# Performance work log

Measured on AMD Instinct MI355X. Metric: run time of the kernel, lower is better.

Reference implementation:

```python
import jax, jax.numpy as jnp
import numpy as np

B, T, D = 2, 2048, 1024
N_HEADS = 16
HEAD_DIM = D // N_HEADS
HIDDEN = 4 * D
LN_EPS = 1e-6  # flax LayerNorm default


def apply_rotary_pos_emb(x, positions):
    # x: (B, T, H, head_dim); positions: (T,)
    head_dim = x.shape[-1]
    inv_freq = 1.0 / 10000 ** (jnp.arange(0, head_dim, 2).astype(jnp.float32) / head_dim)
    freqs = jnp.outer(positions.astype(jnp.float32), inv_freq)  # (T, head_dim//2)
    cos_emb = jnp.cos(freqs)[None, :, None, :]
    sin_emb = jnp.sin(freqs)[None, :, None, :]
    x1 = x[..., : head_dim // 2]
    x2 = x[..., head_dim // 2 :]
    return jnp.concatenate([x1 * cos_emb - x2 * sin_emb,
                            x1 * sin_emb + x2 * cos_emb], axis=-1)


def layernorm(x, scale, bias):
    mu = jnp.mean(x, axis=-1, keepdims=True)
    var = jnp.mean(jnp.square(x - mu), axis=-1, keepdims=True)
    return (x - mu) * jax.lax.rsqrt(var + LN_EPS) * scale + bias


def setup_inputs() -> dict:
    key = jax.random.key(0)
    ks = jax.random.split(key, 8)
    lecun = lambda k, shape: jax.random.normal(k, shape, jnp.float32) * (1.0 / np.sqrt(shape[0]))
    x = jax.random.normal(ks[0], (B, T, D), jnp.float32)
    positions = jnp.arange(T, dtype=jnp.int32)
    mask = jnp.tril(jnp.ones((T, T), dtype=bool))[None, None]  # causal (1,1,T,T)
    return {
        "x": x,
        "positions": positions,
        "mask": mask,
        "ln1_scale": jnp.ones((D,), jnp.float32),
        "ln1_bias": jnp.zeros((D,), jnp.float32),
        "w_qkv": lecun(ks[1], (D, 3 * D)),
        "w_o": lecun(ks[2], (D, D)),
        "ln2_scale": jnp.ones((D,), jnp.float32),
        "ln2_bias": jnp.zeros((D,), jnp.float32),
        "w1": lecun(ks[3], (D, HIDDEN)),
        "b1": jnp.zeros((HIDDEN,), jnp.float32),
        "w2": lecun(ks[4], (HIDDEN, D)),
        "b2": jnp.zeros((D,), jnp.float32),
    }


def reference(x, positions, mask, ln1_scale, ln1_bias, w_qkv, w_o,
              ln2_scale, ln2_bias, w1, b1, w2, b2):
    h = layernorm(x, ln1_scale, ln1_bias)
    qkv = h @ w_qkv  # (B,T,3D)
    qkv = qkv.reshape(B, T, 3, N_HEADS, HEAD_DIM)
    q, k, v = jnp.moveaxis(qkv, 2, 0)  # each (B,T,H,hd)
    q = apply_rotary_pos_emb(q, positions)
    k = apply_rotary_pos_emb(k, positions)
    q = jnp.transpose(q, (0, 2, 1, 3))  # (B,H,T,hd)
    k = jnp.transpose(k, (0, 2, 1, 3))
    v = jnp.transpose(v, (0, 2, 1, 3))
    scale = 1.0 / jnp.sqrt(jnp.float32(HEAD_DIM))
    attn_weights = jnp.einsum('bhqd,bhkd->bhqk', q, k) * scale
    attn_weights = jnp.where(mask, attn_weights, -1e10)
    attn_weights = jax.nn.softmax(attn_weights, axis=-1)
    h = jnp.einsum('bhqk,bhkd->bhqd', attn_weights, v)
    h = jnp.transpose(h, (0, 2, 1, 3)).reshape(B, T, D)
    h = h @ w_o
    x = x + h
    h = layernorm(x, ln2_scale, ln2_bias)
    h = jax.nn.gelu(h @ w1 + b1)  # approximate gelu, matching flax nn.gelu default
    h = h @ w2 + b2
    return x + h
```

## Files before the change

### kernel.cpp

```cpp
#include <hip/hip_runtime.h>


typedef __bf16 bf16_t;
typedef bf16_t bf16x8 __attribute__((ext_vector_type(8)));
typedef float f32x4 __attribute__((ext_vector_type(4)));

#define M_ROWS 4096
#define DMODEL 1024
#define TSEQ   2048
#define NHEAD  16
#define HDIM   64

__device__ __forceinline__ ushort f2bf(float f) {
  union { float f; unsigned u; } v; v.f = f;
  unsigned r = (v.u + 0x7fffu + ((v.u >> 16) & 1u)) >> 16;
  return (ushort)r;
}
__device__ __forceinline__ float bf2f(ushort u) {
  union { unsigned u; float f; } v; v.u = ((unsigned)u) << 16;
  return v.f;
}
__device__ __forceinline__ unsigned cvt_pk_bf16(float a, float b) {
  unsigned r;
  asm("v_cvt_pk_bf16_f32 %0, %1, %2" : "=v"(r) : "v"(a), "v"(b));
  return r;
}
__device__ __forceinline__ void gload_lds16(const void* g, void* l) {
  __builtin_amdgcn_global_load_lds(
      (const __attribute__((address_space(1))) unsigned*)g,
      (__attribute__((address_space(3))) unsigned*)l, 16, 0, 0);
}
__device__ __forceinline__ f32x4 mfma16(bf16x8 a, bf16x8 b, f32x4 c) {
  return __builtin_amdgcn_mfma_f32_16x16x32_bf16(a, b, c, 0, 0, 0);
}
__device__ __forceinline__ float gelu_f(float x) {
  float y = 0.7978845608028654f * (x + 0.044715f * x * x * x);
  float e = __expf(2.0f * y);
  float t = 1.0f - 2.0f / (e + 1.0f);
  return 0.5f * x * (1.0f + t);
}

__global__ __launch_bounds__(256)
void transpose_bf16(const float* __restrict__ src, ushort* __restrict__ dst,
                    int K, int N) {
  __shared__ float t[32][33];
  int n0 = blockIdx.x * 32, k0 = blockIdx.y * 32;
  int tx = threadIdx.x & 31, ty = threadIdx.x >> 5;
#pragma unroll
  for (int i = 0; i < 4; i++) {
    int k = ty + i * 8;
    t[k][tx] = src[(size_t)(k0 + k) * N + n0 + tx];
  }
  __syncthreads();
#pragma unroll
  for (int i = 0; i < 4; i++) {
    int nn = ty + i * 8;
    dst[(size_t)(n0 + nn) * K + k0 + tx] = f2bf(t[tx][nn]);
  }
}

__global__ __launch_bounds__(256)
void ln_kernel(const float* __restrict__ x, const float* __restrict__ sc,
               const float* __restrict__ bi, ushort* __restrict__ out) {
  int row = blockIdx.x;
  int tid = threadIdx.x;
  const float4 v = *(const float4*)&x[(size_t)row * DMODEL + tid * 4];
  float s = v.x + v.y + v.z + v.w;
  float s2 = v.x * v.x + v.y * v.y + v.z * v.z + v.w * v.w;
#pragma unroll
  for (int off = 32; off > 0; off >>= 1) {
    s += __shfl_down(s, off);
    s2 += __shfl_down(s2, off);
  }
  __shared__ float red[8];
  int lane = tid & 63, w = tid >> 6;
  if (lane == 0) { red[w * 2] = s; red[w * 2 + 1] = s2; }
  __syncthreads();
  float S = red[0] + red[2] + red[4] + red[6];
  float S2 = red[1] + red[3] + red[5] + red[7];
  float mu = S * (1.0f / DMODEL);
  float var = S2 * (1.0f / DMODEL) - mu * mu;
  float rs = rsqrtf(var + 1e-6f);
  float4 scv = *(const float4*)&sc[tid * 4];
  float4 biv = *(const float4*)&bi[tid * 4];
  ushort4 o;
  o.x = f2bf((v.x - mu) * rs * scv.x + biv.x);
  o.y = f2bf((v.y - mu) * rs * scv.y + biv.y);
  o.z = f2bf((v.z - mu) * rs * scv.z + biv.z);
  o.w = f2bf((v.w - mu) * rs * scv.w + biv.w);
  *(ushort4*)&out[(size_t)row * DMODEL + tid * 4] = o;
}

__global__ __launch_bounds__(256)
void rope_table(const int* __restrict__ positions, float2* __restrict__ tab) {
  int i = blockIdx.x * 256 + threadIdx.x;
  int t = i >> 5, f = i & 31;
  float inv = __expf(-(float)f * (1.0f / 32.0f) * 9.210340371976184f);
  float a = (float)positions[t] * inv;
  tab[i] = make_float2(cosf(a), sinf(a));
}

__global__ __launch_bounds__(256)
void rope_apply(const ushort* __restrict__ qkv, const float2* __restrict__ tab,
                ushort* __restrict__ Q, ushort* __restrict__ Kd,
                ushort* __restrict__ VT) {
  __shared__ ushort vt[64][66];
  int t0 = blockIdx.x * 64;
  int bh = blockIdx.y;
  int b = bh >> 4, h = bh & 15;
  int f = threadIdx.x & 31, tg = threadIdx.x >> 5;
#pragma unroll
  for (int i = 0; i < 8; i++) {
    int tt = tg * 8 + i;
    int t = t0 + tt;
    const ushort* qr = qkv + (size_t)(b * TSEQ + t) * 3072 + h * 64 + f;
    float2 cs = tab[t * 32 + f];
    float c = cs.x, s = cs.y;
    float q1 = bf2f(qr[0]),    q2 = bf2f(qr[32]);
    float k1 = bf2f(qr[1024]), k2 = bf2f(qr[1056]);
    ushort* Qp = Q + ((size_t)bh * TSEQ + t) * HDIM;
    ushort* Kp = Kd + ((size_t)bh * TSEQ + t) * HDIM;
    Qp[f]      = f2bf(q1 * c - q2 * s);
    Qp[f + 32] = f2bf(q1 * s + q2 * c);
    Kp[f]      = f2bf(k1 * c - k2 * s);
    Kp[f + 32] = f2bf(k1 * s + k2 * c);
    vt[f][tt]      = qr[2048];
    vt[f + 32][tt] = qr[2080];
  }
  __syncthreads();
  int t = threadIdx.x & 63, fg = threadIdx.x >> 6;
  ushort* Vp = VT + (size_t)bh * HDIM * TSEQ + t0 + t;
#pragma unroll
  for (int j = 0; j < 16; j++) {
    int ff = fg * 16 + j;
    Vp[(size_t)ff * TSEQ] = vt[ff][t];
  }
}

__global__ __launch_bounds__(256, 4)
void attn_kernel(const ushort* __restrict__ Q, const ushort* __restrict__ Kd,
                 const ushort* __restrict__ VT, ushort* __restrict__ O) {
  int bh = blockIdx.x;
  int qb = 31 - (int)blockIdx.y;
  int nt = qb + 1;
  int tid = threadIdx.x;
  int lane = tid & 63, w = tid >> 6;
  int qw = qb * 64 + w * 16;
  int lr = lane & 15, lg = lane >> 4;
  int q_abs = qw + lr;

  const ushort* Qb = Q + (size_t)bh * TSEQ * HDIM;
  const ushort* Kb = Kd + (size_t)bh * TSEQ * HDIM;
  const ushort* Vb = VT + (size_t)bh * HDIM * TSEQ;

  __shared__ ushort lK[2][64 * 64];
  __shared__ ushort lV[2][64 * 64];
  __shared__ ushort pt[4][16 * 64];
  ushort* myp = pt[w];

  int srow0 = tid >> 3, sch = tid & 7;

  auto stage = [&](int buf, int kt) {
#pragma unroll
    for (int c = 0; c < 2; c++) {
      int r = c * 32 + srow0;
      int gch = sch ^ (r & 7);
      gload_lds16(Kb + (size_t)(kt + r) * HDIM + gch * 8,
                  &lK[buf][c * 2048 + tid * 8]);
      gload_lds16(Vb + (size_t)r * TSEQ + kt + gch * 8,
                  &lV[buf][c * 2048 + tid * 8]);
    }
  };

  const float QS = 0.125f * 1.44269504088896340736f;
  bf16x8 aq0 = *(const bf16x8*)&Qb[(size_t)q_abs * HDIM + lg * 8];
  bf16x8 aq1 = *(const bf16x8*)&Qb[(size_t)q_abs * HDIM + 32 + lg * 8];
#pragma unroll
  for (int j = 0; j < 8; j++) {
    aq0[j] = (bf16_t)((float)aq0[j] * QS);
    aq1[j] = (bf16_t)((float)aq1[j] * QS);
  }

  float m_run = -1e30f, l_run = 0.0f;
  f32x4 o[4] = {};

  stage(0, 0);
  __syncthreads();

  for (int it = 0; it < nt; ++it) {
    int kt = it * 64;
    int buf = it & 1;
    bool diag = (it == nt - 1);

    if (it + 1 < nt) stage(buf ^ 1, kt + 64);

    f32x4 sa[4];
#pragma unroll
    for (int cb = 0; cb < 4; cb++) {
      int row = cb * 16 + lr;
      const ushort* kp = &lK[buf][row * 64];
      bf16x8 k0 = *(const bf16x8*)(kp + (((lg    ) ^ (row & 7)) << 3));
      bf16x8 k1 = *(const bf16x8*)(kp + (((lg + 4) ^ (row & 7)) << 3));
      f32x4 z = {};
      z = mfma16(k0, aq0, z);
      sa[cb] = mfma16(k1, aq1, z);
    }

    if (diag) {
#pragma unroll
      for (int cb = 0; cb < 4; cb++)
#pragma unroll
        for (int r = 0; r < 4; r++)
          if (kt + cb * 16 + lg * 4 + r > q_abs) sa[cb][r] = -1e30f;
    }

    f32x4 m4;
#pragma unroll
    for (int r = 0; r < 4; r++)
      m4[r] = fmaxf(fmaxf(sa[0][r], sa[1][r]), fmaxf(sa[2][r], sa[3][r]));
    float mx = fmaxf(fmaxf(m4[0], m4[1]), fmaxf(m4[2], m4[3]));
    mx = fmaxf(mx, __shfl_xor(mx, 16, 64));
    mx = fmaxf(mx, __shfl_xor(mx, 32, 64));
    float mn = fmaxf(m_run, mx);
    float rescale = __builtin_amdgcn_exp2f(m_run - mn);
    m_run = mn;

    float ps = 0.0f;
    uint2 pk[4];
#pragma unroll
    for (int cb = 0; cb < 4; cb++) {
      float p0 = __builtin_amdgcn_exp2f(sa[cb][0] - mn);
      float p1 = __builtin_amdgcn_exp2f(sa[cb][1] - mn);
      float p2 = __builtin_amdgcn_exp2f(sa[cb][2] - mn);
      float p3 = __builtin_amdgcn_exp2f(sa[cb][3] - mn);
      ps += (p0 + p1) + (p2 + p3);
      pk[cb].x = cvt_pk_bf16(p0, p1);
      pk[cb].y = cvt_pk_bf16(p2, p3);
    }
    ps += __shfl_xor(ps, 16, 64);
    ps += __shfl_xor(ps, 32, 64);
    l_run = l_run * rescale + ps;

#pragma unroll
    for (int cb = 0; cb < 4; cb++)
      *(uint2*)&myp[lr * 64 + (((cb * 4 + lg) ^ lr) << 2)] = pk[cb];

#pragma unroll
    for (int d = 0; d < 4; d++)
#pragma unroll
      for (int r = 0; r < 4; r++) o[d][r] *= rescale;

    union U8 { uint2 h[2]; bf16x8 v; };
    U8 t0, t1;
    t0.h[0] = *(const uint2*)&myp[lr * 64 + (((lg * 2    ) ^ lr) << 2)];
    t0.h[1] = *(const uint2*)&myp[lr * 64 + (((lg * 2 + 1) ^ lr) << 2)];
    t1.h[0] = *(const uint2*)&myp[lr * 64 + (((8 + lg * 2    ) ^ lr) << 2)];
    t1.h[1] = *(const uint2*)&myp[lr * 64 + (((8 + lg * 2 + 1) ^ lr) << 2)];

#pragma unroll
    for (int d = 0; d < 4; d++) {
      int row = d * 16 + lr;
      const ushort* vp = &lV[buf][row * 64];
      bf16x8 va0 = *(const bf16x8*)(vp + (((lg    ) ^ (row & 7)) << 3));
      bf16x8 va1 = *(const bf16x8*)(vp + (((lg + 4) ^ (row & 7)) << 3));
      o[d] = mfma16(va0, t0.v, o[d]);
      o[d] = mfma16(va1, t1.v, o[d]);
    }

    __syncthreads();
  }

  int b = bh >> 4, h = bh & 15;
  float linv = 1.0f / l_run;
  size_t obase = (size_t)(b * TSEQ + qw + lr) * DMODEL + h * 64;
#pragma unroll
  for (int d = 0; d < 4; d++) {
    uint2 st;
    st.x = cvt_pk_bf16(o[d][0] * linv, o[d][1] * linv);
    st.y = cvt_pk_bf16(o[d][2] * linv, o[d][3] * linv);
    *(uint2*)&O[obase + d * 16 + lg * 4] = st;
  }
}

template <int EPI, int BN>
__global__ __launch_bounds__(256)
void gemm_kernel(const ushort* __restrict__ A, const ushort* __restrict__ Bt,
                 void* __restrict__ Cout, const float* __restrict__ bias,
                 const float* __restrict__ resid, int M, int N, int K,
                 int nbn) {
  constexpr int NF = BN / 32;
  __shared__ ushort lA[128 * 64];
  __shared__ ushort lB[BN * 64];
  int tid = threadIdx.x;
  int lane = tid & 63, w = tid >> 6;
  int wm = w >> 1, wn = w & 1;

  int nwg = gridDim.x;
  int cpx = nwg >> 3;
  int wg = ((int)blockIdx.x & 7) * cpx + ((int)blockIdx.x >> 3);
  int bm = wg / nbn, bn = wg % nbn;

  f32x4 acc[4][NF] = {};

  const ushort* Ab = A + (size_t)bm * 128 * K;
  const ushort* Bb = Bt + (size_t)bn * BN * K;
  int lrow = lane & 15, lg = lane >> 4;
  int srow = tid >> 3, sch = tid & 7;

  for (int k0 = 0; k0 < K; k0 += 64) {
    __syncthreads();
#pragma unroll
    for (int c = 0; c < 4; c++) {
      int r = c * 32 + srow;
      int gch = sch ^ (r & 7);
      gload_lds16(Ab + (size_t)r * K + k0 + gch * 8, &lA[c * 2048 + tid * 8]);
    }
#pragma unroll
    for (int c = 0; c < BN / 32; c++) {
      int r = c * 32 + srow;
      int gch = sch ^ (r & 7);
      gload_lds16(Bb + (size_t)r * K + k0 + gch * 8, &lB[c * 2048 + tid * 8]);
    }
    __syncthreads();

    bf16x8 af[4], bfr[NF];
#pragma unroll
    for (int m = 0; m < 4; m++) {
      int row = wm * 64 + m * 16 + lrow;
      af[m] = *(const bf16x8*)&lA[row * 64 + ((lg ^ (row & 7)) << 3)];
    }
#pragma unroll
    for (int n = 0; n < NF; n++) {
      int row = wn * (BN / 2) + n * 16 + lrow;
      bfr[n] = *(const bf16x8*)&lB[row * 64 + ((lg ^ (row & 7)) << 3)];
    }
#pragma unroll
    for (int m = 0; m < 4; m++)
#pragma unroll
      for (int n = 0; n < NF; n++)
        acc[m][n] = mfma16(af[m], bfr[n], acc[m][n]);
#pragma unroll
    for (int m = 0; m < 4; m++) {
      int row = wm * 64 + m * 16 + lrow;
      af[m] = *(const bf16x8*)&lA[row * 64 + (((4 + lg) ^ (row & 7)) << 3)];
    }
#pragma unroll
    for (int n = 0; n < NF; n++) {
      int row = wn * (BN / 2) + n * 16 + lrow;
      bfr[n] = *(const bf16x8*)&lB[row * 64 + (((4 + lg) ^ (row & 7)) << 3)];
    }
#pragma unroll
    for (int m = 0; m < 4; m++)
#pragma unroll
      for (int n = 0; n < NF; n++)
        acc[m][n] = mfma16(af[m], bfr[n], acc[m][n]);
  }

#pragma unroll
  for (int m = 0; m < 4; m++) {
    int rbase = bm * 128 + wm * 64 + m * 16 + (lane >> 4) * 4;
#pragma unroll
    for (int n = 0; n < NF; n++) {
      int c = bn * BN + wn * (BN / 2) + n * 16 + (lane & 15);
#pragma unroll
      for (int r = 0; r < 4; r++) {
        float v = acc[m][n][r];
        size_t idx = (size_t)(rbase + r) * N + c;
        if constexpr (EPI == 0) {
          ((ushort*)Cout)[idx] = f2bf(v);
        } else if constexpr (EPI == 1) {
          ((float*)Cout)[idx] = v + resid[idx];
        } else if constexpr (EPI == 2) {
          ((ushort*)Cout)[idx] = f2bf(gelu_f(v + bias[c]));
        } else {
          ((float*)Cout)[idx] = v + bias[c] + resid[idx];
        }
      }
    }
  }
}

extern "C" void kernel_launch(void* const* d_in, const int* in_sizes, int n_in,
                              void* d_out, int out_size, void* d_ws,
                              size_t ws_size, hipStream_t stream) {
  const float* x      = (const float*)d_in[0];
  const int* positions = (const int*)d_in[1];
  const float* ln1_s  = (const float*)d_in[3];
  const float* ln1_b  = (const float*)d_in[4];
  const float* w_qkv  = (const float*)d_in[5];
  const float* w_o    = (const float*)d_in[6];
  const float* ln2_s  = (const float*)d_in[7];
  const float* ln2_b  = (const float*)d_in[8];
  const float* w1     = (const float*)d_in[9];
  const float* b1     = (const float*)d_in[10];
  const float* w2     = (const float*)d_in[11];
  const float* b2     = (const float*)d_in[12];
  float* out = (float*)d_out;

  char* ws = (char*)d_ws;
  size_t off = 0;
  auto nxt = [&](size_t bytes) {
    char* p = ws + off;
    off += (bytes + 255) & ~(size_t)255;
    return p;
  };
  ushort* wqkvT = (ushort*)nxt(3072ULL * 1024 * 2);
  ushort* woT   = (ushort*)nxt(1024ULL * 1024 * 2);
  ushort* w1T   = (ushort*)nxt(4096ULL * 1024 * 2);
  ushort* w2T   = (ushort*)nxt(1024ULL * 4096 * 2);
  ushort* h1    = (ushort*)nxt((size_t)M_ROWS * DMODEL * 2);
  ushort* qkv   = (ushort*)nxt((size_t)M_ROWS * 3072 * 2);
  ushort* Qb    = (ushort*)nxt(2ULL * NHEAD * TSEQ * HDIM * 2);
  ushort* Kb    = (ushort*)nxt(2ULL * NHEAD * TSEQ * HDIM * 2);
  ushort* VTb   = (ushort*)nxt(2ULL * NHEAD * TSEQ * HDIM * 2);
  ushort* attn  = (ushort*)nxt((size_t)M_ROWS * DMODEL * 2);
  float*  x2    = (float*)nxt((size_t)M_ROWS * DMODEL * 4);
  ushort* h2    = (ushort*)nxt((size_t)M_ROWS * DMODEL * 2);
  ushort* mid   = (ushort*)nxt((size_t)M_ROWS * 4096 * 2);
  float2* tab   = (float2*)nxt((size_t)TSEQ * 32 * 8);

  transpose_bf16<<<dim3(3072 / 32, 1024 / 32), 256, 0, stream>>>(w_qkv, wqkvT, 1024, 3072);
  transpose_bf16<<<dim3(1024 / 32, 1024 / 32), 256, 0, stream>>>(w_o, woT, 1024, 1024);
  transpose_bf16<<<dim3(4096 / 32, 1024 / 32), 256, 0, stream>>>(w1, w1T, 1024, 4096);
  transpose_bf16<<<dim3(1024 / 32, 4096 / 32), 256, 0, stream>>>(w2, w2T, 4096, 1024);
  rope_table<<<(TSEQ * 32) / 256, 256, 0, stream>>>(positions, tab);
  ln_kernel<<<M_ROWS, 256, 0, stream>>>(x, ln1_s, ln1_b, h1);
  gemm_kernel<0, 128><<<768, 256, 0, stream>>>(h1, wqkvT, qkv, nullptr, nullptr, 4096, 3072, 1024, 24);
  rope_apply<<<dim3(TSEQ / 64, 2 * NHEAD), 256, 0, stream>>>(qkv, tab, Qb, Kb, VTb);
  attn_kernel<<<dim3(32, 32), 256, 0, stream>>>(Qb, Kb, VTb, attn);
  gemm_kernel<1, 64><<<512, 256, 0, stream>>>(attn, woT, x2, nullptr, x, 4096, 1024, 1024, 16);
  ln_kernel<<<M_ROWS, 256, 0, stream>>>(x2, ln2_s, ln2_b, h2);
  gemm_kernel<2, 128><<<1024, 256, 0, stream>>>(h2, w1T, mid, b1, nullptr, 4096, 4096, 1024, 32);
  gemm_kernel<3, 64><<<512, 256, 0, stream>>>(mid, w2T, out, b2, x2, 4096, 1024, 4096, 16);
}
```

Measured before the change: 252.6 us.

## Double-buffer GEMM LDS tiles to overlap global loads with MFMA

The GEMM now uses two LDS buffers. It issues the async global-to-LDS loads for the next K tile right after reading the current tile's fragments, so the loads overlap the MFMA work. All A/B fragments for both K halves are read into registers up front, and s_setprio raises wave priority around the MFMA block. This doubles LDS use per block and raises register pressure, which may lower occupancy.

New measurement: 232.0 us. 1.09x faster.

```diff
diff --git a/kernel.cpp b/kernel.cpp
--- a/kernel.cpp
+++ b/kernel.cpp
@@ -289,8 +289,8 @@
                  const float* __restrict__ resid, int M, int N, int K,
                  int nbn) {
   constexpr int NF = BN / 32;
-  __shared__ ushort lA[128 * 64];
-  __shared__ ushort lB[BN * 64];
+  __shared__ ushort lA[2][128 * 64];
+  __shared__ ushort lB[2][BN * 64];
   int tid = threadIdx.x;
   int lane = tid & 63, w = tid >> 6;
   int wm = w >> 1, wn = w & 1;
@@ -307,53 +307,64 @@
   int lrow = lane & 15, lg = lane >> 4;
   int srow = tid >> 3, sch = tid & 7;
 
-  for (int k0 = 0; k0 < K; k0 += 64) {
-    __syncthreads();
+  auto stage = [&](int buf, int k0) {
 #pragma unroll
     for (int c = 0; c < 4; c++) {
       int r = c * 32 + srow;
       int gch = sch ^ (r & 7);
-      gload_lds16(Ab + (size_t)r * K + k0 + gch * 8, &lA[c * 2048 + tid * 8]);
-    }
-#pragma unroll
-    for (int c = 0; c < BN / 32; c++) {
+      gload_lds16(Ab + (size_t)r * K + k0 + gch * 8,
+                  &lA[buf][c * 2048 + tid * 8]);
+    }
+#pragma unroll
+    for (int c = 0; c < NF; c++) {
       int r = c * 32 + srow;
       int gch = sch ^ (r & 7);
-      gload_lds16(Bb + (size_t)r * K + k0 + gch * 8, &lB[c * 2048 + tid * 8]);
-    }
-    __syncthreads();
-
-    bf16x8 af[4], bfr[NF];
+      gload_lds16(Bb + (size_t)r * K + k0 + gch * 8,
+                  &lB[buf][c * 2048 + tid * 8]);
+    }
+  };
+
+  int nt = K >> 6;
+  stage(0, 0);
+  __syncthreads();
+
+  for (int t = 0; t < nt; ++t) {
+    int cur = t & 1;
+
+    bf16x8 af0[4], af1[4], bf0[NF], bf1[NF];
 #pragma unroll
     for (int m = 0; m < 4; m++) {
       int row = wm * 64 + m * 16 + lrow;
-      af[m] = *(const bf16x8*)&lA[row * 64 + ((lg ^ (row & 7)) << 3)];
+      const ushort* p = &lA[cur][row * 64];
+      af0[m] = *(const bf16x8*)(p + (((lg    ) ^ (row & 7)) << 3));
+      af1[m] = *(const bf16x8*)(p + (((lg + 4) ^ (row & 7)) << 3));
     }
 #pragma unroll
     for (int n = 0; n < NF; n++) {
       int row = wn * (BN / 2) + n * 16 + lrow;
-      bfr[n] = *(const bf16x8*)&lB[row * 64 + ((lg ^ (row & 7)) << 3)];
-    }
+      const ushort* p = &lB[cur][row * 64];
+      bf0[n] = *(const bf16x8*)(p + (((lg    ) ^ (row & 7)) << 3));
+      bf1[n] = *(const bf16x8*)(p + (((lg + 4) ^ (row & 7)) << 3));
+    }
+
+    if (t + 1 < nt) stage(cur ^ 1, (t + 1) << 6);
+
+    __builtin_amdgcn_s_setprio(1);
 #pragma unroll
     for (int m = 0; m < 4; m++)
 #pragma unroll
       for (int n = 0; n < NF; n++)
-        acc[m][n] = mfma16(af[m], bfr[n], acc[m][n]);
-#pragma unroll
-    for (int m = 0; m < 4; m++) {
-      int row = wm * 64 + m * 16 + lrow;
-      af[m] = *(const bf16x8*)&lA[row * 64 + (((4 + lg) ^ (row & 7)) << 3)];
-    }
-#pragma unroll
-    for (int n = 0; n < NF; n++) {
-      int row = wn * (BN / 2) + n * 16 + lrow;
-      bfr[n] = *(const bf16x8*)&lB[row * 64 + (((4 + lg) ^ (row & 7)) << 3)];
-    }
+        acc[m][n] = mfma16(af0[m], bf0[n], acc[m][n]);
 #pragma unroll
     for (int m = 0; m < 4; m++)
 #pragma unroll
       for (int n = 0; n < NF; n++)
-        acc[m][n] = mfma16(af[m], bfr[n], acc[m][n]);
+        acc[m][n] = mfma16(af1[m], bf1[n], acc[m][n]);
+    __builtin_amdgcn_s_setprio(0);
+
+    __builtin_amdgcn_sched_barrier(0);
+    asm volatile("s_waitcnt vmcnt(0)" ::: "memory");
+    __builtin_amdgcn_s_barrier();
   }
 
 #pragma unroll
```
